# Kernel optimization log

Hardware: AMD Instinct MI355X
Metric: run time of the kernel (lower is better)

The kernel has to match this reference:

```python
import jax, jax.numpy as jnp
import numpy as np

B, F, CI, CO, R = 64, 128, 64, 64, 4


def setup_inputs() -> dict:
    key = jax.random.key(0)
    k1, k2 = jax.random.split(key)
    ll = jax.random.normal(k1, (B, F, CI, R), dtype=jnp.float32)
    # WeightedSum requires non-negative weights (no softmax normalization)
    weights = jax.random.uniform(k2, (F, CI, CO, R), dtype=jnp.float32)
    return {"ll": ll, "weights": weights}


def reference(ll, weights):
    # log_weights: log(w) where w > 0, else -inf (zero weights contribute nothing)
    neg_inf = jnp.asarray(-jnp.inf, dtype=weights.dtype)
    log_w = jnp.where(weights > 0, jnp.log(jnp.where(weights > 0, weights, 1.0)), neg_inf)
    # broadcast add: (b,f,ci,1,r) + (1,f,ci,co,r) -> (b,f,ci,co,r), logsumexp over ci
    weighted = ll[:, :, :, None, :] + log_w[None]
    return jax.nn.logsumexp(weighted, axis=2)  # (b, f, co, r)
```

## Files before the change

### kernel.cpp

```cpp
#include <hip/hip_runtime.h>
#include <hip/hip_bf16.h>
#include <math.h>

typedef __attribute__((ext_vector_type(8))) short short8;
typedef __attribute__((ext_vector_type(4))) float f32x4;

#define L2E 1.44269504088896340736f
#define LN2 0.69314718055994530942f

static __device__ __forceinline__ unsigned pk2(float lo, float hi) {
    __hip_bfloat162 h = __float22bfloat162_rn(make_float2(lo, hi));
    union { __hip_bfloat162 h2; unsigned u; } cv; cv.h2 = h;
    return cv.u;
}

__global__ __launch_bounds__(512, 4)
void ws_kernel(const float* __restrict__ ll,
               const float* __restrict__ wt,
               float* __restrict__ out)
{
    __shared__ char smem[8192 + 32768 + 16640];
    float* Obuf = (float*)(smem + 8192 + 32768);

    const int t = threadIdx.x;

    const int i    = blockIdx.x;
    const int tile = (i & 7) * 64 + (i >> 3);
    const int f    = tile >> 2;
    const int b0   = (tile & 3) * 16;

    const float4* llv = (const float4*)ll;
    const int c = t & 31;
    const int b = t >> 5;
    const size_t ebase = (size_t)(b0 + b) * 8192 + (size_t)f * 64 + 2 * c;
    float4 v0 = llv[ebase];
    float4 v1 = llv[ebase + 1];

    const float4* wv = (const float4*)wt;
    const int j  = t & 63;
    const int c8 = t >> 6;
    const size_t wbase = (size_t)f * 4096 + (size_t)(8 * c8) * 64 + j;
    float4 q00 = wv[wbase];
    float4 q01 = wv[wbase + 64];
    float4 q02 = wv[wbase + 128];
    float4 q03 = wv[wbase + 192];
    float4 q10 = wv[wbase + 256];
    float4 q11 = wv[wbase + 320];
    float4 q12 = wv[wbase + 384];
    float4 q13 = wv[wbase + 448];

    {
        float e0x = exp2f(v0.x * L2E), e0y = exp2f(v0.y * L2E),
              e0z = exp2f(v0.z * L2E), e0w = exp2f(v0.w * L2E);
        float e1x = exp2f(v1.x * L2E), e1y = exp2f(v1.y * L2E),
              e1z = exp2f(v1.z * L2E), e1w = exp2f(v1.w * L2E);
        const int off = (c * 4) ^ ((b & 7) << 4);
        char* rowp = smem + b * 128 + off;
        *(unsigned*)(rowp)        = pk2(e0x, e1x);
        *(unsigned*)(rowp + 2048) = pk2(e0y, e1y);
        *(unsigned*)(rowp + 4096) = pk2(e0z, e1z);
        *(unsigned*)(rowp + 6144) = pk2(e0w, e1w);
    }
    {
        const int off = (c8 * 16) ^ ((j & 7) << 4);
        char* rowp = smem + 8192 + j * 128 + off;
        uint4 u;
        u.x = pk2(q00.x, q01.x); u.y = pk2(q02.x, q03.x);
        u.z = pk2(q10.x, q11.x); u.w = pk2(q12.x, q13.x);
        *(uint4*)(rowp) = u;
        u.x = pk2(q00.y, q01.y); u.y = pk2(q02.y, q03.y);
        u.z = pk2(q10.y, q11.y); u.w = pk2(q12.y, q13.y);
        *(uint4*)(rowp + 8192) = u;
        u.x = pk2(q00.z, q01.z); u.y = pk2(q02.z, q03.z);
        u.z = pk2(q10.z, q11.z); u.w = pk2(q12.z, q13.z);
        *(uint4*)(rowp + 16384) = u;
        u.x = pk2(q00.w, q01.w); u.y = pk2(q02.w, q03.w);
        u.z = pk2(q10.w, q11.w); u.w = pk2(q12.w, q13.w);
        *(uint4*)(rowp + 24576) = u;
    }
    __syncthreads();

    const int w   = t >> 6;
    const int l   = t & 63;
    const int r   = w & 3;
    const int coh = w >> 2;
    const int lr  = l & 15;
    const int lg  = l >> 4;
    const char* Ep = smem + r * 2048;
    const char* Wp = smem + 8192 + r * 8192 + coh * 4096;

    f32x4 acc[2] = {{0.f,0.f,0.f,0.f},{0.f,0.f,0.f,0.f}};
    const int swz = (lr & 7) << 4;
    #pragma unroll
    for (int kt = 0; kt < 2; ++kt) {
        const int sb = ((kt * 4 + lg) * 16) ^ swz;
        short8 a0 = *(const short8*)(Ep + lr * 128 + sb);
        short8 w0 = *(const short8*)(Wp + lr * 128 + sb);
        short8 w1 = *(const short8*)(Wp + (lr + 16) * 128 + sb);
        acc[0] = __builtin_amdgcn_mfma_f32_16x16x32_bf16(a0, w0, acc[0], 0, 0, 0);
        acc[1] = __builtin_amdgcn_mfma_f32_16x16x32_bf16(a0, w1, acc[1], 0, 0, 0);
    }

    #pragma unroll
    for (int nt = 0; nt < 2; ++nt) {
        #pragma unroll
        for (int v = 0; v < 4; ++v) {
            Obuf[(lg * 4 + v) * 260 + ((coh * 32 + nt * 16 + lr) * 4 + r)] =
                __log2f(acc[nt][v]) * LN2;
        }
    }
    __syncthreads();

    #pragma unroll
    for (int k = 0; k < 2; ++k) {
        const int bb = w * 2 + k;
        float4 vv = *(const float4*)&Obuf[bb * 260 + l * 4];
        *(float4*)(out + ((size_t)(b0 + bb) * 128 + f) * 256 + l * 4) = vv;
    }
}

extern "C" void kernel_launch(void* const* d_in, const int* in_sizes, int n_in,
                              void* d_out, int out_size, void* d_ws, size_t ws_size,
                              hipStream_t stream)
{
    const float* ll = (const float*)d_in[0];
    const float* wt = (const float*)d_in[1];
    float* out = (float*)d_out;
    hipLaunchKernelGGL(ws_kernel, dim3(512), dim3(512), 0, stream, ll, wt, out);
}
```

Measured before the change: 10.74 us.

## Process two batch tiles per block to reuse weight tile and halve grid

```diff
diff --git a/kernel.cpp b/kernel.cpp
--- a/kernel.cpp
+++ b/kernel.cpp
@@ -14,40 +14,44 @@
     return cv.u;
 }
 
-__global__ __launch_bounds__(512, 4)
+__global__ __launch_bounds__(512, 2)
 void ws_kernel(const float* __restrict__ ll,
                const float* __restrict__ wt,
                float* __restrict__ out)
 {
-    __shared__ char smem[8192 + 32768 + 16640];
-    float* Obuf = (float*)(smem + 8192 + 32768);
+    __shared__ char smem[65536];
+    float* Obuf = (float*)(smem + 49152);
 
     const int t = threadIdx.x;
 
-    const int i    = blockIdx.x;
-    const int tile = (i & 7) * 64 + (i >> 3);
-    const int f    = tile >> 2;
-    const int b0   = (tile & 3) * 16;
+    const int i  = blockIdx.x;
+    const int x  = i & 7;
+    const int k  = i >> 3;
+    const int f  = x * 16 + (k >> 1);
+    const int b0 = (k & 1) * 32;
 
     const float4* llv = (const float4*)ll;
     const int c = t & 31;
     const int b = t >> 5;
-    const size_t ebase = (size_t)(b0 + b) * 8192 + (size_t)f * 64 + 2 * c;
-    float4 v0 = llv[ebase];
-    float4 v1 = llv[ebase + 1];
+    const size_t e0 = (size_t)(b0 + b) * 8192 + (size_t)f * 64 + 2 * c;
+    float4 v0 = llv[e0];
+    float4 v1 = llv[e0 + 1];
 
     const float4* wv = (const float4*)wt;
     const int j  = t & 63;
     const int c8 = t >> 6;
-    const size_t wbase = (size_t)f * 4096 + (size_t)(8 * c8) * 64 + j;
-    float4 q00 = wv[wbase];
-    float4 q01 = wv[wbase + 64];
-    float4 q02 = wv[wbase + 128];
-    float4 q03 = wv[wbase + 192];
-    float4 q10 = wv[wbase + 256];
-    float4 q11 = wv[wbase + 320];
-    float4 q12 = wv[wbase + 384];
-    float4 q13 = wv[wbase + 448];
+    const size_t wb = (size_t)f * 4096 + (size_t)(8 * c8) * 64 + j;
+    float4 q00 = wv[wb];
+    float4 q01 = wv[wb + 64];
+    float4 q02 = wv[wb + 128];
+    float4 q03 = wv[wb + 192];
+    float4 q10 = wv[wb + 256];
+    float4 q11 = wv[wb + 320];
+    float4 q12 = wv[wb + 384];
+    float4 q13 = wv[wb + 448];
+
+    float4 u0 = llv[e0 + 131072];
+    float4 u1 = llv[e0 + 131073];
 
     {
         float e0x = exp2f(v0.x * L2E), e0y = exp2f(v0.y * L2E),
@@ -63,7 +67,7 @@
     }
     {
         const int off = (c8 * 16) ^ ((j & 7) << 4);
-        char* rowp = smem + 8192 + j * 128 + off;
+        char* rowp = smem + 16384 + j * 128 + off;
         uint4 u;
         u.x = pk2(q00.x, q01.x); u.y = pk2(q02.x, q03.x);
         u.z = pk2(q10.x, q11.x); u.w = pk2(q12.x, q13.x);
@@ -86,36 +90,95 @@
     const int coh = w >> 2;
     const int lr  = l & 15;
     const int lg  = l >> 4;
-    const char* Ep = smem + r * 2048;
-    const char* Wp = smem + 8192 + r * 8192 + coh * 4096;
+    const int swz = (lr & 7) << 4;
+    const char* Wp = smem + 16384 + r * 8192 + coh * 4096;
 
-    f32x4 acc[2] = {{0.f,0.f,0.f,0.f},{0.f,0.f,0.f,0.f}};
-    const int swz = (lr & 7) << 4;
+    f32x4 acc0[2] = {{0.f,0.f,0.f,0.f},{0.f,0.f,0.f,0.f}};
+    {
+        const char* Ep = smem + r * 2048;
+        #pragma unroll
+        for (int kt = 0; kt < 2; ++kt) {
+            const int sb = ((kt * 4 + lg) * 16) ^ swz;
+            short8 a0 = *(const short8*)(Ep + lr * 128 + sb);
+            short8 w0 = *(const short8*)(Wp + lr * 128 + sb);
+            short8 w1 = *(const short8*)(Wp + (lr + 16) * 128 + sb);
+            acc0[0] = __builtin_amdgcn_mfma_f32_16x16x32_bf16(a0, w0, acc0[0], 0, 0, 0);
+            acc0[1] = __builtin_amdgcn_mfma_f32_16x16x32_bf16(a0, w1, acc0[1], 0, 0, 0);
+        }
+    }
     #pragma unroll
-    for (int kt = 0; kt < 2; ++kt) {
-        const int sb = ((kt * 4 + lg) * 16) ^ swz;
-        short8 a0 = *(const short8*)(Ep + lr * 128 + sb);
-        short8 w0 = *(const short8*)(Wp + lr * 128 + sb);
-        short8 w1 = *(const short8*)(Wp + (lr + 16) * 128 + sb);
-        acc[0] = __builtin_amdgcn_mfma_f32_16x16x32_bf16(a0, w0, acc[0], 0, 0, 0);
-        acc[1] = __builtin_amdgcn_mfma_f32_16x16x32_bf16(a0, w1, acc[1], 0, 0, 0);
+    for (int nt = 0; nt < 2; ++nt) {
+        #pragma unroll
+        for (int v = 0; v < 4; ++v) {
+            const int bl = lg * 4 + v;
+            const int co = (coh * 32 + nt * 16 + lr) ^ (lg << 3);
+            Obuf[r * 1024 + bl * 64 + co] = __log2f(acc0[nt][v]) * LN2;
+        }
     }
+    {
+        float e0x = exp2f(u0.x * L2E), e0y = exp2f(u0.y * L2E),
+              e0z = exp2f(u0.z * L2E), e0w = exp2f(u0.w * L2E);
+        float e1x = exp2f(u1.x * L2E), e1y = exp2f(u1.y * L2E),
+              e1z = exp2f(u1.z * L2E), e1w = exp2f(u1.w * L2E);
+        const int off = (c * 4) ^ ((b & 7) << 4);
+        char* rowp = smem + 8192 + b * 128 + off;
+        *(unsigned*)(rowp)        = pk2(e0x, e1x);
+        *(unsigned*)(rowp + 2048) = pk2(e0y, e1y);
+        *(unsigned*)(rowp + 4096) = pk2(e0z, e1z);
+        *(unsigned*)(rowp + 6144) = pk2(e0w, e1w);
+    }
+    __syncthreads();
+
+    #pragma unroll
+    for (int kk = 0; kk < 2; ++kk) {
+        const int bb = w * 2 + kk;
+        const int sx = (bb >> 2) << 3;
+        const int idx = bb * 64 + (l ^ sx);
+        float4 vv;
+        vv.x = Obuf[idx];
+        vv.y = Obuf[idx + 1024];
+        vv.z = Obuf[idx + 2048];
+        vv.w = Obuf[idx + 3072];
+        *(float4*)(out + ((size_t)(b0 + bb) * 128 + f) * 256 + l * 4) = vv;
+    }
+
+    f32x4 acc1[2] = {{0.f,0.f,0.f,0.f},{0.f,0.f,0.f,0.f}};
+    {
+        const char* Ep = smem + 8192 + r * 2048;
+        #pragma unroll
+        for (int kt = 0; kt < 2; ++kt) {
+            const int sb = ((kt * 4 + lg) * 16) ^ swz;
+            short8 a0 = *(const short8*)(Ep + lr * 128 + sb);
+            short8 w0 = *(const short8*)(Wp + lr * 128 + sb);
+            short8 w1 = *(const short8*)(Wp + (lr + 16) * 128 + sb);
+            acc1[0] = __builtin_amdgcn_mfma_f32_16x16x32_bf16(a0, w0, acc1[0], 0, 0, 0);
+            acc1[1] = __builtin_amdgcn_mfma_f32_16x16x32_bf16(a0, w1, acc1[1], 0, 0, 0);
+        }
+    }
+    __syncthreads();
 
     #pragma unroll
     for (int nt = 0; nt < 2; ++nt) {
         #pragma unroll
         for (int v = 0; v < 4; ++v) {
-            Obuf[(lg * 4 + v) * 260 + ((coh * 32 + nt * 16 + lr) * 4 + r)] =
-                __log2f(acc[nt][v]) * LN2;
+            const int bl = lg * 4 + v;
+            const int co = (coh * 32 + nt * 16 + lr) ^ (lg << 3);
+            Obuf[r * 1024 + bl * 64 + co] = __log2f(acc1[nt][v]) * LN2;
         }
     }
     __syncthreads();
 
     #pragma unroll
-    for (int k = 0; k < 2; ++k) {
-        const int bb = w * 2 + k;
-        float4 vv = *(const float4*)&Obuf[bb * 260 + l * 4];
-        *(float4*)(out + ((size_t)(b0 + bb) * 128 + f) * 256 + l * 4) = vv;
+    for (int kk = 0; kk < 2; ++kk) {
+        const int bb = w * 2 + kk;
+        const int sx = (bb >> 2) << 3;
+        const int idx = bb * 64 + (l ^ sx);
+        float4 vv;
+        vv.x = Obuf[idx];
+        vv.y = Obuf[idx + 1024];
+        vv.z = Obuf[idx + 2048];
+        vv.w = Obuf[idx + 3072];
+        *(float4*)(out + ((size_t)(b0 + 16 + bb) * 128 + f) * 256 + l * 4) = vv;
     }
 }
 
@@ -126,5 +189,5 @@
     const float* ll = (const float*)d_in[0];
     const float* wt = (const float*)d_in[1];
     float* out = (float*)d_out;
-    hipLaunchKernelGGL(ws_kernel, dim3(512), dim3(512), 0, stream, ll, wt, out);
+    hipLaunchKernelGGL(ws_kernel, dim3(256), dim3(512), 0, stream, ll, wt, out);
 }
```

Result: no change. 10.63 us (-1.0%).
